# Kernel tuning notes

Hardware: AMD Instinct MI355X
Metric: run time of the kernel (lower is better)

Reference implementation:

```python
import jax, jax.numpy as jnp
import numpy as np

D = 768
H = 16
DH = D // H  # 48


def setup_inputs() -> dict:
    key = jax.random.key(0)
    ks = jax.random.split(key, 7)
    s = 0.02
    x = jax.random.normal(ks[0], (4, 2048, D), dtype=jnp.float32)
    # weights stored as (in, out); torch Linear is y = x @ W.T + b
    W_qkv = jax.random.normal(ks[1], (D, 3 * D), dtype=jnp.float32) * s
    b_qkv = jax.random.normal(ks[2], (3 * D,), dtype=jnp.float32) * s
    W_o = jax.random.normal(ks[3], (D, D), dtype=jnp.float32) * s
    b_o = jax.random.normal(ks[4], (D,), dtype=jnp.float32) * s
    W_p = jax.random.normal(ks[5], (D, D), dtype=jnp.float32) * s
    b_p = jax.random.normal(ks[6], (D,), dtype=jnp.float32) * s
    return {"x": x, "W_qkv": W_qkv, "b_qkv": b_qkv, "W_o": W_o, "b_o": b_o, "W_p": W_p, "b_p": b_p}


def reference(x, W_qkv, b_qkv, W_o, b_o, W_p, b_p):
    b, n, _ = x.shape
    qkv = x @ W_qkv + b_qkv                     # (b, n, 3*D)
    # reshape to (b, n, H, 3*DH) as in torch, then chunk last dim into q,k,v
    # -> per-head interleaved layout [q_h | k_h | v_h]
    qkv = qkv.reshape(b, n, H, 3, DH).transpose(0, 2, 1, 3, 4)  # (b, H, n, 3, DH)
    q, k, v = qkv[..., 0, :], qkv[..., 1, :], qkv[..., 2, :]    # (b, H, n, DH)
    alpha = jnp.einsum("bhqd,bhkd->bhqk", q, k) / jnp.sqrt(jnp.float32(DH))
    alpha = jax.nn.softmax(alpha, axis=-1)      # dropout: eval mode (identity)
    out = jnp.einsum("bhqk,bhkd->bhqd", alpha, v)
    out = out.transpose(0, 2, 1, 3).reshape(b, n, D)
    out = out @ W_o + b_o
    out = out @ W_p + b_p
    return out
```

## Files before the change

kernel.cpp:

```cpp
#include <hip/hip_runtime.h>

#define DEV __device__ __forceinline__

typedef __attribute__((ext_vector_type(4))) float f32x4;
typedef __attribute__((ext_vector_type(8))) short bf16x8;
typedef __attribute__((ext_vector_type(4))) short bf16x4;
typedef __attribute__((ext_vector_type(4))) unsigned int u32x4;

DEV short f2bf(float f) {
  union { float f; unsigned u; } c; c.f = f;
  unsigned r = c.u + 0x7FFFu + ((c.u >> 16) & 1u);
  return (short)(r >> 16);
}

DEV unsigned cvtpk(float lo, float hi) {
  unsigned r;
  asm("v_cvt_pk_bf16_f32 %0, %1, %2" : "=v"(r) : "v"(lo), "v"(hi));
  return r;
}

DEV float exp2r(float x) { return __builtin_amdgcn_exp2f(x); }

DEV void gl_lds16(short* lds, const short* g) {
  __builtin_amdgcn_global_load_lds(
      (__attribute__((address_space(1))) void*)(void*)g,
      (__attribute__((address_space(3))) void*)lds, 16, 0, 0);
}

DEV int xcd_swz(int orig, int nwg) {
  int q = nwg >> 3, r = nwg & 7;
  int xcd = orig & 7, idx = orig >> 3;
  return (xcd < r ? xcd * (q + 1) : r * (q + 1) + (xcd - r) * q) + idx;
}

__global__ __launch_bounds__(256) void k_cvt2(const float* __restrict__ in1, short* __restrict__ out1,
                                              int nb1, const float* __restrict__ in2, short* __restrict__ out2) {
  int b = blockIdx.x;
  const float* in = in1; short* out = out1;
  if (b >= nb1) { in = in2; out = out2; b -= nb1; }
  int i = b * 256 + threadIdx.x;
  float4 v = reinterpret_cast<const float4*>(in)[i];
  bf16x4 o;
  o[0] = f2bf(v.x); o[1] = f2bf(v.y); o[2] = f2bf(v.z); o[3] = f2bf(v.w);
  reinterpret_cast<bf16x4*>(out)[i] = o;
}

__global__ __launch_bounds__(256) void k_tcvt(const float* __restrict__ W, short* __restrict__ WT,
                                              int Kd, int Nd) {
  __shared__ float t[32][33];
  int nb = blockIdx.x * 32, kb = blockIdx.y * 32;
  int tx = threadIdx.x, ty = threadIdx.y;
#pragma unroll
  for (int i = ty; i < 32; i += 8) t[i][tx] = W[(long)(kb + i) * Nd + nb + tx];
  __syncthreads();
#pragma unroll
  for (int i = ty; i < 32; i += 8) WT[(long)(nb + i) * Kd + kb + tx] = f2bf(t[tx][i]);
}

__global__ __launch_bounds__(256) void k_bias(const float* __restrict__ bo, const float* __restrict__ bp,
                                              const float* __restrict__ Wp, float* __restrict__ bc) {
  int j = blockIdx.x * 256 + threadIdx.x;
  int k0 = blockIdx.y * 48;
  float s = 0.f;
#pragma unroll
  for (int k = 0; k < 48; ++k) s += bo[k0 + k] * Wp[(long)(k0 + k) * 768 + j];
  if (blockIdx.y == 0) s += bp[j];
  atomicAdd(&bc[j], s);
}

template <int MODE>
__global__ __launch_bounds__(512, 2) void k_gemm256(
    const short* __restrict__ A, const short* __restrict__ BT, const float* __restrict__ bias,
    float* __restrict__ Cf,
    short* __restrict__ Qp, short* __restrict__ Kp, short* __restrict__ VT,
    int N, int K) {
  __shared__ short As[2][256 * 32];
  __shared__ short Bs[2][256 * 32];
  const int tid = threadIdx.x;
  const int w = tid >> 6, lane = tid & 63;
  const int lr = lane & 15, g = lane >> 4;
  const int row4 = lane >> 2;
  const int cs8 = ((lane & 3) ^ ((lane >> 3) & 3)) * 8;

  const int nbx = gridDim.x;
  int lin = blockIdx.y * nbx + blockIdx.x;
  lin = xcd_swz(lin, nbx * gridDim.y);
  const int bx = lin % nbx, by = lin / nbx;
  const int m0 = by * 256, n0 = bx * 256;
  const int wm = (w >> 1) * 64, wn = (w & 1) * 128;

  f32x4 acc[4][8];
#pragma unroll
  for (int i = 0; i < 4; ++i)
#pragma unroll
    for (int j = 0; j < 8; ++j)
#pragma unroll
      for (int r = 0; r < 4; ++r) acc[i][j][r] = 0.f;

  const short* Ab = A + (long)m0 * K;
  const short* Bb = BT + (long)n0 * K;
  const int nk = K >> 5;

  auto STAGE = [&](int s, int kt) {
    const int k0 = kt << 5;
    int r0 = w * 16;
    gl_lds16(&As[s][r0 * 32],         Ab + (long)(r0 + row4) * K + k0 + cs8);
    gl_lds16(&As[s][(128 + r0) * 32], Ab + (long)(128 + r0 + row4) * K + k0 + cs8);
    gl_lds16(&Bs[s][r0 * 32],         Bb + (long)(r0 + row4) * K + k0 + cs8);
    gl_lds16(&Bs[s][(128 + r0) * 32], Bb + (long)(128 + r0 + row4) * K + k0 + cs8);
  };

  STAGE(0, 0);

  for (int kt = 0; kt < nk; ++kt) {
    asm volatile("s_waitcnt vmcnt(0)" ::: "memory");
    __builtin_amdgcn_s_barrier();
    if (kt + 1 < nk) STAGE((kt + 1) & 1, kt + 1);

    const short* AsC = As[kt & 1];
    const short* BsC = Bs[kt & 1];
    bf16x8 af[4], bf[8];
#pragma unroll
    for (int mi = 0; mi < 4; ++mi) {
      int r = wm + mi * 16 + lr;
      int c = g ^ ((r >> 1) & 3);
      af[mi] = *reinterpret_cast<const bf16x8*>(AsC + r * 32 + c * 8);
    }
#pragma unroll
    for (int nj = 0; nj < 8; ++nj) {
      int r = wn + nj * 16 + lr;
      int c = g ^ ((r >> 1) & 3);
      bf[nj] = *reinterpret_cast<const bf16x8*>(BsC + r * 32 + c * 8);
    }
    __builtin_amdgcn_s_setprio(1);
#pragma unroll
    for (int mi = 0; mi < 4; ++mi)
#pragma unroll
      for (int nj = 0; nj < 8; ++nj)
        acc[mi][nj] = __builtin_amdgcn_mfma_f32_16x16x32_bf16(af[mi], bf[nj], acc[mi][nj], 0, 0, 0);
    __builtin_amdgcn_s_setprio(0);
  }

#pragma unroll
  for (int nj = 0; nj < 8; ++nj) {
    int col = n0 + wn + nj * 16 + lr;
    float bv = bias[col];
    if (MODE == 0) {
      int h = col / 144;
      int rem = col - h * 144;
      int s = rem / 48;
      int d = rem - s * 48;
#pragma unroll
      for (int mi = 0; mi < 4; ++mi)
#pragma unroll
        for (int r = 0; r < 4; ++r) {
          int row = m0 + wm + mi * 16 + g * 4 + r;
          float val = acc[mi][nj][r] + bv;
          int b = row >> 11, n = row & 2047;
          int bh = (b << 4) + h;
          if (s == 0) {
            long o = ((long)(bh * 2048 + n)) * 64 + d;
            Qp[o] = f2bf(val * 0.20823051649867783f);
            if (d < 16) Qp[o + 48] = 0;
          } else if (s == 1) {
            long o = ((long)(bh * 2048 + n)) * 64 + d;
            Kp[o] = f2bf(val);
            if (d < 16) Kp[o + 48] = 0;
          } else {
            VT[((long)(bh * 48 + d)) * 2048 + n] = f2bf(val);
          }
        }
    } else {
#pragma unroll
      for (int mi = 0; mi < 4; ++mi)
#pragma unroll
        for (int r = 0; r < 4; ++r) {
          int row = m0 + wm + mi * 16 + g * 4 + r;
          Cf[(long)row * N + col] = acc[mi][nj][r] + bv;
        }
    }
  }
}

template <int MODE>
__global__ __launch_bounds__(256) void k_gemm(
    const short* __restrict__ A, const short* __restrict__ BT, const float* __restrict__ bias,
    short* __restrict__ Cb, float* __restrict__ Cf, int M, int N, int K) {
  __shared__ short As[3][128 * 32];
  __shared__ short Bs[3][128 * 32];
  const int tid = threadIdx.x;
  const int w = tid >> 6, lane = tid & 63;
  const int lr = lane & 15, g = lane >> 4;

  const int nbx = gridDim.x;
  int lin = blockIdx.y * nbx + blockIdx.x;
  lin = xcd_swz(lin, nbx * gridDim.y);
  const int bx = lin % nbx, by = lin / nbx;
  const int m0 = by * 128, n0 = bx * 128;
  const int wm = (w >> 1) * 64, wn = (w & 1) * 64;

  f32x4 acc[4][4];
#pragma unroll
  for (int i = 0; i < 4; ++i)
#pragma unroll
    for (int j = 0; j < 4; ++j)
#pragma unroll
      for (int r = 0; r < 4; ++r) acc[i][j][r] = 0.f;

  const short* Ab = A + (long)m0 * K;
  const short* Bb = BT + (long)n0 * K;
  const int row_s = tid >> 2;
  const int c_s = tid & 3;
  const int nk = K >> 5;

  auto STAGE = [&](int b, int kt) {
    const int k0 = kt << 5;
#pragma unroll
    for (int i = 0; i < 2; ++i) {
      int row = row_s + i * 64;
      int cs = c_s ^ ((row >> 1) & 3);
      gl_lds16(&As[b][(i * 256 + w * 64) * 8], Ab + (long)row * K + k0 + cs * 8);
      gl_lds16(&Bs[b][(i * 256 + w * 64) * 8], Bb + (long)row * K + k0 + cs * 8);
    }
  };

  STAGE(0, 0);
  STAGE(1, 1);

  for (int kt = 0; kt < nk; ++kt) {
    if (kt < nk - 1) asm volatile("s_waitcnt vmcnt(4)" ::: "memory");
    else             asm volatile("s_waitcnt vmcnt(0)" ::: "memory");
    __builtin_amdgcn_s_barrier();

    if (kt + 2 < nk) STAGE((kt + 2) % 3, kt + 2);

    const short* AsC = As[kt % 3];
    const short* BsC = Bs[kt % 3];
    bf16x8 af[4], bf[4];
#pragma unroll
    for (int mi = 0; mi < 4; ++mi) {
      int r = wm + mi * 16 + lr;
      int c = g ^ ((r >> 1) & 3);
      af[mi] = *reinterpret_cast<const bf16x8*>(AsC + r * 32 + c * 8);
    }
#pragma unroll
    for (int nj = 0; nj < 4; ++nj) {
      int r = wn + nj * 16 + lr;
      int c = g ^ ((r >> 1) & 3);
      bf[nj] = *reinterpret_cast<const bf16x8*>(BsC + r * 32 + c * 8);
    }
    __builtin_amdgcn_s_setprio(1);
#pragma unroll
    for (int mi = 0; mi < 4; ++mi)
#pragma unroll
      for (int nj = 0; nj < 4; ++nj)
        acc[mi][nj] = __builtin_amdgcn_mfma_f32_16x16x32_bf16(af[mi], bf[nj], acc[mi][nj], 0, 0, 0);
    __builtin_amdgcn_s_setprio(0);
  }

#pragma unroll
  for (int nj = 0; nj < 4; ++nj) {
    int col = n0 + wn + nj * 16 + lr;
    float bv = (MODE == 3) ? 0.f : bias[col];
#pragma unroll
    for (int mi = 0; mi < 4; ++mi)
#pragma unroll
      for (int r = 0; r < 4; ++r) {
        int row = m0 + wm + mi * 16 + g * 4 + r;
        float val = acc[mi][nj][r] + bv;
        if (MODE == 2) Cf[(long)row * N + col] = val;
        else           Cb[(long)row * N + col] = f2bf(val);
      }
  }
}

__global__ __launch_bounds__(256, 4) void k_attn(const short* __restrict__ Q, const short* __restrict__ K,
                                                 const short* __restrict__ VT, short* __restrict__ AO) {
  const int tid = threadIdx.x, w = tid >> 6, lane = tid & 63;
  const int lr = lane & 15, g = lane >> 4;
  const int orig = blockIdx.x;
  const int logical = (orig & 7) * 128 + (orig >> 3);
  const int bh = logical >> 4;
  const int q0 = (logical & 15) * 128 + w * 32;

  const short* Qh = Q + (long)bh * 2048 * 64;
  const short* Kh = K + (long)bh * 2048 * 64;
  const short* VTh = VT + (long)bh * 48 * 2048;

  __shared__ short Ks[2][64 * 64];
  __shared__ short Vs[2][48 * 64];

  const int r_l = lane >> 3, c_l = lane & 7;
  const int gc8 = (c_l ^ r_l) * 8;

  bf16x8 bq0 = *reinterpret_cast<const bf16x8*>(Qh + (q0 + lr) * 64 + g * 8);
  bf16x8 bq1 = *reinterpret_cast<const bf16x8*>(Qh + (q0 + lr) * 64 + 32 + g * 8);
  bf16x8 bq2 = *reinterpret_cast<const bf16x8*>(Qh + (q0 + 16 + lr) * 64 + g * 8);
  bf16x8 bq3 = *reinterpret_cast<const bf16x8*>(Qh + (q0 + 16 + lr) * 64 + 32 + g * 8);

  bf16x8 vones;
#pragma unroll
  for (int i = 0; i < 8; ++i) vones[i] = (short)0x3F80;

  f32x4 accA[3], accB[3];
#pragma unroll
  for (int df = 0; df < 3; ++df)
#pragma unroll
    for (int r = 0; r < 4; ++r) { accA[df][r] = 0.f; accB[df][r] = 0.f; }
  f32x4 acclA = {0.f, 0.f, 0.f, 0.f}, acclB = {0.f, 0.f, 0.f, 0.f};

  const short* kg = Kh + (long)(w * 8 + r_l) * 64 + gc8;
  const short* vg = VTh + (long)(w * 8 + r_l) * 2048 + gc8;

  auto STAGE = [&](int b) {
    gl_lds16(&Ks[b][w * 512], kg);
    gl_lds16(&Ks[b][(w + 4) * 512], kg + 2048);
    gl_lds16(&Vs[b][w * 512], vg);
    if (w < 2) gl_lds16(&Vs[b][(w + 4) * 512], vg + 65536);
  };

  STAGE(0);
  kg += 4096; vg += 64;
  asm volatile("s_waitcnt vmcnt(0)" ::: "memory");
  __syncthreads();

  const int sw = lr & 7;
  const int goff = (g & 1) * 4;
  const int ghalf = g >> 1;

  for (int t = 0; t < 32; ++t) {
    const int cur = t & 1;
    if (t < 31) {
      STAGE(cur ^ 1);
      kg += 4096; vg += 64;
    }

    const short* KsC = Ks[cur];
    const short* VsC = Vs[cur];

    f32x4 stA[4], stB[4];
    __builtin_amdgcn_s_setprio(1);
#pragma unroll
    for (int kf = 0; kf < 4; ++kf) {
      const short* kr = KsC + (kf * 16 + lr) * 64;
      bf16x8 a0 = *reinterpret_cast<const bf16x8*>(kr + (g ^ sw) * 8);
      bf16x8 a1 = *reinterpret_cast<const bf16x8*>(kr + ((4 + g) ^ sw) * 8);
      f32x4 sA = {0.f, 0.f, 0.f, 0.f}, sB = {0.f, 0.f, 0.f, 0.f};
      sA = __builtin_amdgcn_mfma_f32_16x16x32_bf16(a0, bq0, sA, 0, 0, 0);
      sB = __builtin_amdgcn_mfma_f32_16x16x32_bf16(a0, bq2, sB, 0, 0, 0);
      sA = __builtin_amdgcn_mfma_f32_16x16x32_bf16(a1, bq1, sA, 0, 0, 0);
      sB = __builtin_amdgcn_mfma_f32_16x16x32_bf16(a1, bq3, sB, 0, 0, 0);
      stA[kf] = sA; stB[kf] = sB;
    }
    __builtin_amdgcn_s_setprio(0);

#pragma unroll
    for (int kf = 0; kf < 4; ++kf)
#pragma unroll
      for (int r = 0; r < 4; ++r) {
        stA[kf][r] = exp2r(stA[kf][r]);
        stB[kf][r] = exp2r(stB[kf][r]);
      }

    __builtin_amdgcn_s_setprio(1);
#pragma unroll
    for (int ks = 0; ks < 2; ++ks) {
      u32x4 bwA, bwB;
      bwA[0] = cvtpk(stA[2 * ks][0], stA[2 * ks][1]);
      bwA[1] = cvtpk(stA[2 * ks][2], stA[2 * ks][3]);
      bwA[2] = cvtpk(stA[2 * ks + 1][0], stA[2 * ks + 1][1]);
      bwA[3] = cvtpk(stA[2 * ks + 1][2], stA[2 * ks + 1][3]);
      bwB[0] = cvtpk(stB[2 * ks][0], stB[2 * ks][1]);
      bwB[1] = cvtpk(stB[2 * ks][2], stB[2 * ks][3]);
      bwB[2] = cvtpk(stB[2 * ks + 1][0], stB[2 * ks + 1][1]);
      bwB[3] = cvtpk(stB[2 * ks + 1][2], stB[2 * ks + 1][3]);
      bf16x8 bpA = __builtin_bit_cast(bf16x8, bwA);
      bf16x8 bpB = __builtin_bit_cast(bf16x8, bwB);
      const int off_lo = ((ks * 4 + ghalf) ^ sw) * 8 + goff;
      const int off_hi = ((ks * 4 + 2 + ghalf) ^ sw) * 8 + goff;
      acclA = __builtin_amdgcn_mfma_f32_16x16x32_bf16(vones, bpA, acclA, 0, 0, 0);
      acclB = __builtin_amdgcn_mfma_f32_16x16x32_bf16(vones, bpB, acclB, 0, 0, 0);
#pragma unroll
      for (int df = 0; df < 3; ++df) {
        const short* vbase = VsC + (df * 16 + lr) * 64;
        union { bf16x8 v; bf16x4 h[2]; } av;
        av.h[0] = *reinterpret_cast<const bf16x4*>(vbase + off_lo);
        av.h[1] = *reinterpret_cast<const bf16x4*>(vbase + off_hi);
        accA[df] = __builtin_amdgcn_mfma_f32_16x16x32_bf16(av.v, bpA, accA[df], 0, 0, 0);
        accB[df] = __builtin_amdgcn_mfma_f32_16x16x32_bf16(av.v, bpB, accB[df], 0, 0, 0);
      }
    }
    __builtin_amdgcn_s_setprio(0);

    asm volatile("s_waitcnt vmcnt(0)" ::: "memory");
    __syncthreads();
  }

  int b = bh >> 4, h = bh & 15;
  float invA = 1.f / acclA[0];
  float invB = 1.f / acclB[0];
  long rowA = ((long)((b << 11) + q0 + lr)) * 768 + h * 48;
  long rowB = ((long)((b << 11) + q0 + 16 + lr)) * 768 + h * 48;
#pragma unroll
  for (int df = 0; df < 3; ++df) {
    bf16x4 oA, oB;
#pragma unroll
    for (int r = 0; r < 4; ++r) { oA[r] = f2bf(accA[df][r] * invA); oB[r] = f2bf(accB[df][r] * invB); }
    *reinterpret_cast<bf16x4*>(AO + rowA + df * 16 + g * 4) = oA;
    *reinterpret_cast<bf16x4*>(AO + rowB + df * 16 + g * 4) = oB;
  }
}

extern "C" void kernel_launch(void* const* d_in, const int* in_sizes, int n_in,
                              void* d_out, int out_size, void* d_ws, size_t ws_size,
                              hipStream_t stream) {
  const float* x    = (const float*)d_in[0];
  const float* Wqkv = (const float*)d_in[1];
  const float* bqkv = (const float*)d_in[2];
  const float* Wo   = (const float*)d_in[3];
  const float* bo   = (const float*)d_in[4];
  const float* Wp   = (const float*)d_in[5];
  const float* bp   = (const float*)d_in[6];

  char* ws = (char*)d_ws;
  short* xb    = (short*)(ws + 0);
  short* WqkvT = (short*)(ws + 12582912);
  short* Wob   = (short*)(ws + 16121856);
  short* WpT   = (short*)(ws + 17301504);
  short* Qp    = (short*)(ws + 18481152);
  short* Kp    = (short*)(ws + 35258368);
  short* VT    = (short*)(ws + 52035584);
  short* AO    = (short*)(ws + 64618496);
  short* WoWpT = (short*)(ws + 2097152);
  float* bc    = (float*)(ws + 4194304);

  k_cvt2<<<6720, 256, 0, stream>>>(x, xb, 6144, Wo, Wob);
  k_tcvt<<<dim3(72, 24), dim3(32, 8), 0, stream>>>(Wqkv, WqkvT, 768, 2304);
  k_tcvt<<<dim3(24, 24), dim3(32, 8), 0, stream>>>(Wp, WpT, 768, 768);

  k_gemm256<0><<<dim3(9, 32), 512, 0, stream>>>(xb, WqkvT, bqkv, nullptr,
                                                Qp, Kp, VT, 2304, 768);
  k_gemm<3><<<dim3(6, 6), 256, 0, stream>>>(WpT, Wob, nullptr, WoWpT, nullptr, 768, 768, 768);
  hipMemsetAsync(bc, 0, 768 * sizeof(float), stream);
  k_bias<<<dim3(3, 16), 256, 0, stream>>>(bo, bp, Wp, bc);

  k_attn<<<1024, 256, 0, stream>>>(Qp, Kp, VT, AO);
  k_gemm256<2><<<dim3(3, 32), 512, 0, stream>>>(AO, WoWpT, bc, (float*)d_out,
                                                nullptr, nullptr, nullptr, 768, 768);
}
```

Baseline: 222.8 us.

## Fuse fp32-to-bf16 conversion of x into QKV GEMM and retile kernels

Removes the separate pass that converted x to bf16: the QKV GEMM now loads fp32 rows into registers, packs them to bf16 and writes them into swizzled LDS, using 128x128 tiles with 256 threads in place of 256x256 tiles. The attention kernel moves to 512-thread blocks covering 256 queries each, so a K/V tile staged once is shared by twice as many query rows. The output projection now uses the generic 128-tile GEMM. These changes drop a full write and reread of the bf16 copy of x, but the A tile is staged through registers with an extra wait and barrier per k-step, and the grid and occupancy shapes change.

```diff
diff --git a/kernel.cpp b/kernel.cpp
--- a/kernel.cpp
+++ b/kernel.cpp
@@ -6,6 +6,7 @@
 typedef __attribute__((ext_vector_type(8))) short bf16x8;
 typedef __attribute__((ext_vector_type(4))) short bf16x4;
 typedef __attribute__((ext_vector_type(4))) unsigned int u32x4;
+typedef __attribute__((ext_vector_type(2))) unsigned int u32x2;
 
 DEV short f2bf(float f) {
   union { float f; unsigned u; } c; c.f = f;
@@ -33,12 +34,8 @@
   return (xcd < r ? xcd * (q + 1) : r * (q + 1) + (xcd - r) * q) + idx;
 }
 
-__global__ __launch_bounds__(256) void k_cvt2(const float* __restrict__ in1, short* __restrict__ out1,
-                                              int nb1, const float* __restrict__ in2, short* __restrict__ out2) {
-  int b = blockIdx.x;
-  const float* in = in1; short* out = out1;
-  if (b >= nb1) { in = in2; out = out2; b -= nb1; }
-  int i = b * 256 + threadIdx.x;
+__global__ __launch_bounds__(256) void k_cvt(const float* __restrict__ in, short* __restrict__ out) {
+  int i = blockIdx.x * 256 + threadIdx.x;
   float4 v = reinterpret_cast<const float4*>(in)[i];
   bf16x4 o;
   o[0] = f2bf(v.x); o[1] = f2bf(v.y); o[2] = f2bf(v.z); o[3] = f2bf(v.w);
@@ -68,58 +65,83 @@
   atomicAdd(&bc[j], s);
 }
 
-template <int MODE>
-__global__ __launch_bounds__(512, 2) void k_gemm256(
-    const short* __restrict__ A, const short* __restrict__ BT, const float* __restrict__ bias,
-    float* __restrict__ Cf,
-    short* __restrict__ Qp, short* __restrict__ Kp, short* __restrict__ VT,
-    int N, int K) {
-  __shared__ short As[2][256 * 32];
-  __shared__ short Bs[2][256 * 32];
+__global__ __launch_bounds__(256) void k_gemmA(
+    const float* __restrict__ X, const short* __restrict__ BT, const float* __restrict__ bias,
+    short* __restrict__ Qp, short* __restrict__ Kp, short* __restrict__ VT, int K) {
+  __shared__ short As[2][128 * 32];
+  __shared__ short Bs[2][128 * 32];
   const int tid = threadIdx.x;
   const int w = tid >> 6, lane = tid & 63;
   const int lr = lane & 15, g = lane >> 4;
-  const int row4 = lane >> 2;
-  const int cs8 = ((lane & 3) ^ ((lane >> 3) & 3)) * 8;
 
   const int nbx = gridDim.x;
   int lin = blockIdx.y * nbx + blockIdx.x;
   lin = xcd_swz(lin, nbx * gridDim.y);
   const int bx = lin % nbx, by = lin / nbx;
-  const int m0 = by * 256, n0 = bx * 256;
-  const int wm = (w >> 1) * 64, wn = (w & 1) * 128;
-
-  f32x4 acc[4][8];
+  const int m0 = by * 128, n0 = bx * 128;
+  const int wm = (w >> 1) * 64, wn = (w & 1) * 64;
+
+  f32x4 acc[4][4];
 #pragma unroll
   for (int i = 0; i < 4; ++i)
 #pragma unroll
-    for (int j = 0; j < 8; ++j)
+    for (int j = 0; j < 4; ++j)
 #pragma unroll
       for (int r = 0; r < 4; ++r) acc[i][j][r] = 0.f;
 
-  const short* Ab = A + (long)m0 * K;
+  const float* Xb = X + (long)m0 * K;
   const short* Bb = BT + (long)n0 * K;
   const int nk = K >> 5;
 
-  auto STAGE = [&](int s, int kt) {
+  const int arow = tid >> 3;
+  const int gi = tid & 7;
+  const int brow = tid >> 2;
+  const int bcs = tid & 3;
+
+  float4 avreg[4];
+  auto LOAD_A = [&](int kt) {
+#pragma unroll
+    for (int j = 0; j < 4; ++j)
+      avreg[j] = *reinterpret_cast<const float4*>(Xb + (long)(arow + j * 32) * K + (kt << 5) + gi * 4);
+  };
+  auto WRITE_A = [&](int s) {
+#pragma unroll
+    for (int j = 0; j < 4; ++j) {
+      int row = arow + j * 32;
+      int sc = (gi >> 1) ^ ((row >> 1) & 3);
+      int goff = (sc * 2 + (gi & 1)) * 4;
+      u32x2 pk;
+      pk[0] = cvtpk(avreg[j].x, avreg[j].y);
+      pk[1] = cvtpk(avreg[j].z, avreg[j].w);
+      *reinterpret_cast<u32x2*>(&As[s][row * 32 + goff]) = pk;
+    }
+  };
+  auto STAGE_B = [&](int s, int kt) {
     const int k0 = kt << 5;
-    int r0 = w * 16;
-    gl_lds16(&As[s][r0 * 32],         Ab + (long)(r0 + row4) * K + k0 + cs8);
-    gl_lds16(&As[s][(128 + r0) * 32], Ab + (long)(128 + r0 + row4) * K + k0 + cs8);
-    gl_lds16(&Bs[s][r0 * 32],         Bb + (long)(r0 + row4) * K + k0 + cs8);
-    gl_lds16(&Bs[s][(128 + r0) * 32], Bb + (long)(128 + r0 + row4) * K + k0 + cs8);
+#pragma unroll
+    for (int i = 0; i < 2; ++i) {
+      int row = brow + i * 64;
+      int cs = bcs ^ ((row >> 1) & 3);
+      gl_lds16(&Bs[s][(i * 256 + w * 64) * 8], Bb + (long)row * K + k0 + cs * 8);
+    }
   };
 
-  STAGE(0, 0);
+  LOAD_A(0);
+  STAGE_B(0, 0);
+  asm volatile("s_waitcnt vmcnt(0)" ::: "memory");
+  WRITE_A(0);
+  __syncthreads();
 
   for (int kt = 0; kt < nk; ++kt) {
-    asm volatile("s_waitcnt vmcnt(0)" ::: "memory");
-    __builtin_amdgcn_s_barrier();
-    if (kt + 1 < nk) STAGE((kt + 1) & 1, kt + 1);
-
-    const short* AsC = As[kt & 1];
-    const short* BsC = Bs[kt & 1];
-    bf16x8 af[4], bf[8];
+    const int cur = kt & 1;
+    if (kt + 1 < nk) {
+      LOAD_A(kt + 1);
+      STAGE_B(cur ^ 1, kt + 1);
+    }
+
+    const short* AsC = As[cur];
+    const short* BsC = Bs[cur];
+    bf16x8 af[4], bf[4];
 #pragma unroll
     for (int mi = 0; mi < 4; ++mi) {
       int r = wm + mi * 16 + lr;
@@ -127,7 +149,7 @@
       af[mi] = *reinterpret_cast<const bf16x8*>(AsC + r * 32 + c * 8);
     }
 #pragma unroll
-    for (int nj = 0; nj < 8; ++nj) {
+    for (int nj = 0; nj < 4; ++nj) {
       int r = wn + nj * 16 + lr;
       int c = g ^ ((r >> 1) & 3);
       bf[nj] = *reinterpret_cast<const bf16x8*>(BsC + r * 32 + c * 8);
@@ -136,49 +158,45 @@
 #pragma unroll
     for (int mi = 0; mi < 4; ++mi)
 #pragma unroll
-      for (int nj = 0; nj < 8; ++nj)
+      for (int nj = 0; nj < 4; ++nj)
         acc[mi][nj] = __builtin_amdgcn_mfma_f32_16x16x32_bf16(af[mi], bf[nj], acc[mi][nj], 0, 0, 0);
     __builtin_amdgcn_s_setprio(0);
-  }
-
-#pragma unroll
-  for (int nj = 0; nj < 8; ++nj) {
+
+    if (kt + 1 < nk) {
+      asm volatile("s_waitcnt vmcnt(0)" ::: "memory");
+      WRITE_A(cur ^ 1);
+    }
+    __syncthreads();
+  }
+
+#pragma unroll
+  for (int nj = 0; nj < 4; ++nj) {
     int col = n0 + wn + nj * 16 + lr;
     float bv = bias[col];
-    if (MODE == 0) {
-      int h = col / 144;
-      int rem = col - h * 144;
-      int s = rem / 48;
-      int d = rem - s * 48;
-#pragma unroll
-      for (int mi = 0; mi < 4; ++mi)
-#pragma unroll
-        for (int r = 0; r < 4; ++r) {
-          int row = m0 + wm + mi * 16 + g * 4 + r;
-          float val = acc[mi][nj][r] + bv;
-          int b = row >> 11, n = row & 2047;
-          int bh = (b << 4) + h;
-          if (s == 0) {
-            long o = ((long)(bh * 2048 + n)) * 64 + d;
-            Qp[o] = f2bf(val * 0.20823051649867783f);
-            if (d < 16) Qp[o + 48] = 0;
-          } else if (s == 1) {
-            long o = ((long)(bh * 2048 + n)) * 64 + d;
-            Kp[o] = f2bf(val);
-            if (d < 16) Kp[o + 48] = 0;
-          } else {
-            VT[((long)(bh * 48 + d)) * 2048 + n] = f2bf(val);
-          }
+    int h = col / 144;
+    int rem = col - h * 144;
+    int s = rem / 48;
+    int d = rem - s * 48;
+#pragma unroll
+    for (int mi = 0; mi < 4; ++mi)
+#pragma unroll
+      for (int r = 0; r < 4; ++r) {
+        int row = m0 + wm + mi * 16 + g * 4 + r;
+        float val = acc[mi][nj][r] + bv;
+        int b = row >> 11, n = row & 2047;
+        int bh = (b << 4) + h;
+        if (s == 0) {
+          long o = ((long)(bh * 2048 + n)) * 64 + d;
+          Qp[o] = f2bf(val * 0.20823051649867783f);
+          if (d < 16) Qp[o + 48] = 0;
+        } else if (s == 1) {
+          long o = ((long)(bh * 2048 + n)) * 64 + d;
+          Kp[o] = f2bf(val);
+          if (d < 16) Kp[o + 48] = 0;
+        } else {
+          VT[((long)(bh * 48 + d)) * 2048 + n] = f2bf(val);
         }
-    } else {
-#pragma unroll
-      for (int mi = 0; mi < 4; ++mi)
-#pragma unroll
-        for (int r = 0; r < 4; ++r) {
-          int row = m0 + wm + mi * 16 + g * 4 + r;
-          Cf[(long)row * N + col] = acc[mi][nj][r] + bv;
-        }
-    }
+      }
   }
 }
 
@@ -274,14 +292,14 @@
   }
 }
 
-__global__ __launch_bounds__(256, 4) void k_attn(const short* __restrict__ Q, const short* __restrict__ K,
+__global__ __launch_bounds__(512, 4) void k_attn(const short* __restrict__ Q, const short* __restrict__ K,
                                                  const short* __restrict__ VT, short* __restrict__ AO) {
   const int tid = threadIdx.x, w = tid >> 6, lane = tid & 63;
   const int lr = lane & 15, g = lane >> 4;
   const int orig = blockIdx.x;
-  const int logical = (orig & 7) * 128 + (orig >> 3);
-  const int bh = logical >> 4;
-  const int q0 = (logical & 15) * 128 + w * 32;
+  const int logical = (orig & 7) * 64 + (orig >> 3);
+  const int bh = logical >> 3;
+  const int q0 = (logical & 7) * 256 + w * 32;
 
   const short* Qh = Q + (long)bh * 2048 * 64;
   const short* Kh = K + (long)bh * 2048 * 64;
@@ -314,9 +332,7 @@
 
   auto STAGE = [&](int b) {
     gl_lds16(&Ks[b][w * 512], kg);
-    gl_lds16(&Ks[b][(w + 4) * 512], kg + 2048);
-    gl_lds16(&Vs[b][w * 512], vg);
-    if (w < 2) gl_lds16(&Vs[b][(w + 4) * 512], vg + 65536);
+    if (w < 6) gl_lds16(&Vs[b][w * 512], vg);
   };
 
   STAGE(0);
@@ -423,7 +439,6 @@
   const float* bp   = (const float*)d_in[6];
 
   char* ws = (char*)d_ws;
-  short* xb    = (short*)(ws + 0);
   short* WqkvT = (short*)(ws + 12582912);
   short* Wob   = (short*)(ws + 16121856);
   short* WpT   = (short*)(ws + 17301504);
@@ -434,17 +449,16 @@
   short* WoWpT = (short*)(ws + 2097152);
   float* bc    = (float*)(ws + 4194304);
 
-  k_cvt2<<<6720, 256, 0, stream>>>(x, xb, 6144, Wo, Wob);
   k_tcvt<<<dim3(72, 24), dim3(32, 8), 0, stream>>>(Wqkv, WqkvT, 768, 2304);
   k_tcvt<<<dim3(24, 24), dim3(32, 8), 0, stream>>>(Wp, WpT, 768, 768);
-
-  k_gemm256<0><<<dim3(9, 32), 512, 0, stream>>>(xb, WqkvT, bqkv, nullptr,
-                                                Qp, Kp, VT, 2304, 768);
+  k_cvt<<<576, 256, 0, stream>>>(Wo, Wob);
+
+  k_gemmA<<<dim3(18, 64), 256, 0, stream>>>(x, WqkvT, bqkv, Qp, Kp, VT, 768);
+
   k_gemm<3><<<dim3(6, 6), 256, 0, stream>>>(WpT, Wob, nullptr, WoWpT, nullptr, 768, 768, 768);
   hipMemsetAsync(bc, 0, 768 * sizeof(float), stream);
   k_bias<<<dim3(3, 16), 256, 0, stream>>>(bo, bp, Wp, bc);
 
-  k_attn<<<1024, 256, 0, stream>>>(Qp, Kp, VT, AO);
-  k_gemm256<2><<<dim3(3, 32), 512, 0, stream>>>(AO, WoWpT, bc, (float*)d_out,
-                                                nullptr, nullptr, nullptr, 768, 768);
-}
+  k_attn<<<512, 512, 0, stream>>>(Qp, Kp, VT, AO);
+  k_gemm<2><<<dim3(6, 64), 256, 0, stream>>>(AO, WoWpT, bc, nullptr, (float*)d_out, 8192, 768, 768);
+}
```

Result: faster. 187.8 us (-15.7%).
